# Performance work log

Measured on AMD Instinct MI355X. Metric: run time of the kernel, lower is better.

Reference implementation:

```python
import jax, jax.numpy as jnp
import numpy as np

DG = 4   # deformable groups
KK = 9   # 3x3 kernel
BN_EPS = 1e-5


def setup_inputs() -> dict:
    key = jax.random.key(0)
    ks = jax.random.split(key, 4)
    B, C, H, W = 4, 64, 160, 160
    fea = jax.random.normal(ks[0], (B, C, H, W), jnp.float32)
    # 1x1 offset conv (no bias) + BN (eval-mode running stats)
    w_off = jax.random.normal(ks[1], (C, C), jnp.float32) * 0.05
    bn_gamma = jnp.ones((C,), jnp.float32)
    bn_beta = jnp.zeros((C,), jnp.float32)
    bn_mean = jnp.zeros((C,), jnp.float32)
    bn_var = jnp.ones((C,), jnp.float32)
    # conv_offset_mask: 3x3 conv -> 3*DG*KK = 108 channels (o1, o2, mask)
    w_com = jax.random.normal(ks[2], (3 * DG * KK, C, 3, 3), jnp.float32) * 0.02
    b_com = jnp.zeros((3 * DG * KK,), jnp.float32)
    # modulated deformable conv main weight/bias
    w_dcn = jax.random.normal(ks[3], (C, C, 3, 3), jnp.float32) * 0.05
    b_dcn = jnp.zeros((C,), jnp.float32)
    return dict(fea=fea, w_off=w_off, bn_gamma=bn_gamma, bn_beta=bn_beta,
                bn_mean=bn_mean, bn_var=bn_var, w_com=w_com, b_com=b_com,
                w_dcn=w_dcn, b_dcn=b_dcn)


def _forward(fea, w_off, bn_gamma, bn_beta, bn_mean, bn_var, w_com, b_com, w_dcn, b_dcn):
    B, C, H, W = fea.shape
    Cg = C // DG
    # ---- offset branch: 1x1 conv + BN (eval) ----
    off_feat = jnp.einsum('bihw,oi->bohw', fea, w_off)
    inv = bn_gamma / jnp.sqrt(bn_var + BN_EPS)
    off_feat = off_feat * inv[None, :, None, None] + (bn_beta - bn_mean * inv)[None, :, None, None]
    # ---- conv_offset_mask 3x3, pad 1 ----
    com = jax.lax.conv_general_dilated(
        off_feat, w_com, (1, 1), ((1, 1), (1, 1)),
        dimension_numbers=('NCHW', 'OIHW', 'NCHW')) + b_com[None, :, None, None]
    o1, o2, m = jnp.split(com, 3, axis=1)                 # each [B, DG*KK, H, W]
    off = jnp.concatenate([o1, o2], axis=1).reshape(B, DG, KK, 2, H, W)
    dy = off[:, :, :, 0]                                  # [B, DG, KK, H, W]
    dx = off[:, :, :, 1]
    mask = jax.nn.sigmoid(m).reshape(B, DG, KK, H, W)
    # ---- sampling locations (stride=1, pad=1, dil=1) ----
    ky = (jnp.arange(KK) // 3 - 1).astype(fea.dtype)
    kx = (jnp.arange(KK) % 3 - 1).astype(fea.dtype)
    py = dy + ky[None, None, :, None, None] + jnp.arange(H, dtype=fea.dtype)[None, None, None, :, None]
    px = dx + kx[None, None, :, None, None] + jnp.arange(W, dtype=fea.dtype)[None, None, None, None, :]
    # ---- bilinear gather with zero padding outside ----
    fea_g = fea.reshape(B, DG, Cg, H * W)
    y0 = jnp.floor(py)
    x0 = jnp.floor(px)
    wy = py - y0
    wx = px - x0
    y0i = y0.astype(jnp.int32)
    x0i = x0.astype(jnp.int32)

    def corner(yi, xi, wgt):
        valid = ((yi >= 0) & (yi < H) & (xi >= 0) & (xi < W)).astype(fea.dtype)
        idx = jnp.clip(yi, 0, H - 1) * W + jnp.clip(xi, 0, W - 1)  # [B,DG,KK,H,W]
        v = jnp.take_along_axis(fea_g, idx.reshape(B, DG, 1, KK * H * W), axis=3)
        v = v.reshape(B, DG, Cg, KK, H, W)
        return v * (wgt * valid)[:, :, None]

    val = (corner(y0i,     x0i,     (1 - wy) * (1 - wx))
         + corner(y0i,     x0i + 1, (1 - wy) * wx)
         + corner(y0i + 1, x0i,     wy * (1 - wx))
         + corner(y0i + 1, x0i + 1, wy * wx))
    val = val * mask[:, :, None]                          # modulated im2col [B,DG,Cg,KK,H,W]
    # ---- deformable conv contraction + bias, relu, residual ----
    out = jnp.einsum('bgckhw,ogck->bohw', val, w_dcn.reshape(C, DG, Cg, KK)) + b_dcn[None, :, None, None]
    return fea + jax.nn.relu(out)


def reference(fea, w_off, bn_gamma, bn_beta, bn_mean, bn_var, w_com, b_com, w_dcn, b_dcn):
    return _forward(fea, w_off, bn_gamma, bn_beta, bn_mean, bn_var, w_com, b_com, w_dcn, b_dcn)
```

## Files before the change

kernel.cpp:

```cpp
#include <hip/hip_runtime.h>
#include <math.h>

#define Hc 160
#define Wc 160
#define HWc (Hc*Wc)
#define Cc 64
#define COMC 108

typedef __attribute__((ext_vector_type(8))) short short8;
typedef __attribute__((ext_vector_type(4))) float f32x4;
typedef __attribute__((ext_vector_type(2))) float f32x2;

__device__ inline short f2bf(float f) {
    union { float f; unsigned u; } v; v.f = f;
    unsigned r = (v.u + 0x7FFFu + ((v.u >> 16) & 1u)) >> 16;
    return (short)r;
}
__device__ inline float bf2f(short s) {
    union { unsigned u; float f; } v; v.u = ((unsigned)(unsigned short)s) << 16; return v.f;
}
__device__ inline float bflo(unsigned u) {
    union { unsigned u; float f; } v; v.u = u << 16; return v.f;
}
__device__ inline float bfhi(unsigned u) {
    union { unsigned u; float f; } v; v.u = u & 0xFFFF0000u; return v.f;
}
__device__ inline f32x2 bf2x2(unsigned u) {
    union { unsigned u; float f; } lo, hi;
    lo.u = u << 16; hi.u = u & 0xFFFF0000u;
    return (f32x2){lo.f, hi.f};
}
__device__ inline unsigned packbf_fast(float lo, float hi) {
    union { float f; unsigned u; } a, b; a.f = lo; b.f = hi;
    return ((a.u + 0x8000u) >> 16) | ((b.u + 0x8000u) & 0xFFFF0000u);
}

__global__ __launch_bounds__(256) void k_prep2(
    const float* __restrict__ w_off,
    const float* __restrict__ bn_g, const float* __restrict__ bn_b,
    const float* __restrict__ bn_m, const float* __restrict__ bn_v,
    const float* __restrict__ w_com, const float* __restrict__ w_dcn,
    short* __restrict__ wof_frag, float* __restrict__ shift,
    short* __restrict__ wfrag, short* __restrict__ wdT)
{
    const int t = blockIdx.x * 256 + threadIdx.x;
    if (t < 64) {
        const float scale = bn_g[t] * __frsqrt_rn(bn_v[t] + 1e-5f);
        shift[t] = bn_b[t] - bn_m[t] * scale;
    }
    if (t < 4096) {
        const int j = t & 7;
        const int lane = (t >> 3) & 63;
        const int v = t >> 9;
        const int s = v & 1, m = v >> 1;
        const int o = m*16 + (lane & 15);
        const int i = s*32 + (lane >> 4)*8 + j;
        const float scale = bn_g[o] * __frsqrt_rn(bn_v[o] + 1e-5f);
        wof_frag[t] = f2bf(w_off[o*64 + i] * scale);
    }
    if (t < 64512) {
        const int j = t & 7;
        const int lane = (t >> 3) & 63;
        const int v = t >> 9;
        const int s = v % 18, m = v / 18;
        const int kk = s >> 1, h = s & 1;
        const int o = m*16 + (lane & 15);
        const int i = h*32 + (lane >> 4)*8 + j;
        wfrag[t] = (o < COMC) ? f2bf(w_com[(o*64 + i)*9 + kk]) : (short)0;
    }
    if (t < 36864) {
        const int j = t & 7;
        const int lane = (t >> 3) & 63;
        const int v = t >> 9;
        const int s = v % 18, m = v / 18;
        const int o = m*16 + (lane & 15);
        const int q = s*32 + (lane >> 4)*8 + j;
        const int ch = q & 63, kk = q >> 6;
        wdT[t] = f2bf(w_dcn[o*576 + ch*9 + kk]);
    }
}

__global__ __launch_bounds__(256) void k_off3(
    const float* __restrict__ fea, const short* __restrict__ wof_frag,
    const float* __restrict__ shift,
    short* __restrict__ off_bf, short* __restrict__ fea_gp)
{
    __shared__ short sm[64][72];
    const int b = blockIdx.y;
    const int w = threadIdx.x >> 6, lane = threadIdx.x & 63;
    const int n = lane & 15, g = lane >> 4;
    const int p = blockIdx.x * 64 + w * 16 + n;
    const float* f = fea + (size_t)b * Cc * HWc + p;

    short8 bfrag[2];
    #pragma unroll
    for (int s = 0; s < 2; ++s) {
        #pragma unroll
        for (int j = 0; j < 8; ++j)
            bfrag[s][j] = f2bf(f[(size_t)(s*32 + g*8 + j) * HWc]);
        const int gg = s*2 + (g >> 1);
        *(short8*)&fea_gp[(((size_t)b*4 + gg)*HWc + p)*16 + (g & 1)*8] = bfrag[s];
    }

    f32x4 acc[4];
    #pragma unroll
    for (int m = 0; m < 4; ++m) acc[m] = (f32x4){0.f, 0.f, 0.f, 0.f};
    #pragma unroll
    for (int s = 0; s < 2; ++s) {
        #pragma unroll
        for (int m = 0; m < 4; ++m) {
            const short8 afrag = *(const short8*)&wof_frag[((m*2 + s)*64 + lane)*8];
            acc[m] = __builtin_amdgcn_mfma_f32_16x16x32_bf16(afrag, bfrag[s], acc[m], 0, 0, 0);
        }
    }
    #pragma unroll
    for (int m = 0; m < 4; ++m) {
        #pragma unroll
        for (int r = 0; r < 4; ++r) {
            const int o = m*16 + g*4 + r;
            sm[w*16 + n][o] = f2bf(acc[m][r] + shift[o]);
        }
    }
    __syncthreads();
    for (int q = threadIdx.x; q < 512; q += 256) {
        const int pl = q >> 3, sc = q & 7;
        *(uint4*)&off_bf[((size_t)(b * HWc) + blockIdx.x*64 + pl)*64 + sc*8] =
            *(const uint4*)&sm[pl][sc*8];
    }
}

#define SWZ(px, sc) ((sc) ^ ((px) & 7))

__global__ __launch_bounds__(256) void k_com6(
    const short* __restrict__ off_bf, const short* __restrict__ wfrag,
    const float* __restrict__ b_com, short* __restrict__ com_rec)
{
    __shared__ short smem[14336];
    const int seg = blockIdx.x;
    const int yb  = blockIdx.y * 4;
    const int b   = blockIdx.z;
    const int x0  = seg * 32;
    const int tid = threadIdx.x;

    for (int c = tid; c < 1632; c += 256) {
        const int r   = c / 272;
        const int rem = c - r * 272;
        const int px  = rem >> 3;
        const int sc  = rem & 7;
        const int gy  = yb + r - 1;
        const int gx  = x0 + px - 1;
        uint4 vv = make_uint4(0u, 0u, 0u, 0u);
        if ((unsigned)gy < (unsigned)Hc && (unsigned)gx < (unsigned)Wc)
            vv = *(const uint4*)&off_bf[(((size_t)b * HWc + gy * Wc + gx) << 6) + (sc << 3)];
        *(uint4*)&smem[((r*34 + px)*8 + SWZ(px, sc)) * 8] = vv;
    }
    __syncthreads();

    const int w    = tid >> 6;
    const int lane = tid & 63;
    const int n15  = lane & 15;
    const int g    = lane >> 4;
    const int m0   = w * 2;
    const int nm   = (w == 3) ? 1 : 2;

    f32x4 acc[2][8];
    #pragma unroll
    for (int mm = 0; mm < 2; ++mm)
        #pragma unroll
        for (int t = 0; t < 8; ++t) acc[mm][t] = (f32x4){0.f, 0.f, 0.f, 0.f};

    #pragma unroll
    for (int kk = 0; kk < 9; ++kk) {
        #pragma unroll
        for (int h = 0; h < 2; ++h) {
            const int s = kk*2 + h;
            const int slot = h*4 + g;
            short8 bf[8];
            #pragma unroll
            for (int t = 0; t < 8; ++t) {
                const int r  = t >> 1, xt = t & 1;
                const int ry = r + kk/3;
                const int rx = xt*16 + n15 + (kk % 3);
                bf[t] = *(const short8*)&smem[((ry*34 + rx)*8 + SWZ(rx, slot)) * 8];
            }
            #pragma unroll
            for (int mm = 0; mm < 2; ++mm) {
                if (mm < nm) {
                    const short8 afrag =
                        *(const short8*)&wfrag[(((m0+mm)*18 + s)*64 + lane)*8];
                    #pragma unroll
                    for (int t = 0; t < 8; ++t)
                        acc[mm][t] = __builtin_amdgcn_mfma_f32_16x16x32_bf16(
                            afrag, bf[t], acc[mm][t], 0, 0, 0);
                }
            }
        }
    }
    __syncthreads();

    #pragma unroll
    for (int mm = 0; mm < 2; ++mm) {
        if (mm < nm) {
            #pragma unroll
            for (int r4 = 0; r4 < 4; ++r4) {
                const int oc = (m0+mm)*16 + g*4 + r4;
                if (oc < COMC) {
                    int pos;
                    if (oc < 72) pos = oc;
                    else { const int q = oc - 72; pos = 72 + (q/9)*10 + (q - (q/9)*9); }
                    const float bo = b_com[oc];
                    #pragma unroll
                    for (int t = 0; t < 8; ++t) {
                        const int r = t >> 1, xt = t & 1;
                        smem[(r*32 + xt*16 + n15)*112 + pos] = f2bf(acc[mm][t][r4] + bo);
                    }
                }
            }
        }
    }
    __syncthreads();

    for (int c = tid; c < 1792; c += 256) {
        const int pr = c / 14, ch = c - pr * 14;
        const int r = pr >> 5, pxl = pr & 31;
        const int p = (yb + r) * Wc + x0 + pxl;
        *(uint4*)&com_rec[((size_t)b * HWc + p)*112 + ch*8] = *(const uint4*)&smem[pr*112 + ch*8];
    }
}

__global__ __launch_bounds__(256, 4) void k_dcn8(
    const float* __restrict__ fea, const short* __restrict__ com_rec,
    const short* __restrict__ fea_gp, const short* __restrict__ wdT,
    const float* __restrict__ b_dcn, float* __restrict__ out)
{
    __shared__ short stage_s[10752];
    __shared__ short val_s[9216];
    const int nx = gridDim.x;
    int bid = blockIdx.x;
    bid = (bid & 7) * (nx >> 3) + (bid >> 3);
    const int b = blockIdx.y;
    const int base = bid * 16;
    const int ty = base / Wc;
    const int tx = base - ty * Wc;
    const int tid = threadIdx.x;
    const int w = tid >> 6, lane = tid & 63;

    const int eo = tid >> 2, eq = tid & 3;
    const size_t egb = ((size_t)b * Cc + eo) * HWc + base + eq*4;
    const float4 fv = *(const float4*)&fea[egb];

    const int ns = (lane < 16) ? 3 : 2;
    int sk[3], sg[3], sl[3];
    unsigned sdydx[3]; float smk[3];
    #pragma unroll
    for (int i = 0; i < 3; ++i) {
        const int s = w*144 + i*64 + lane;
        sk[i] = s >> 6; sg[i] = (s >> 4) & 3; sl[i] = s & 15;
        if (i < ns) {
            const short* crp = &com_rec[((size_t)b * HWc + base + sl[i]) * 112];
            sdydx[i] = *(const unsigned*)&crp[sg[i]*18 + 2*sk[i]];
            smk[i]   = bf2f(crp[72 + sg[i]*10 + sk[i]]);
        }
    }

    for (int cq = tid; cq < 1344; cq += 256) {
        const int g = cq / 336, rem = cq - g*336;
        const int r = rem / 48, rem2 = rem - r*48;
        const int c = rem2 >> 1, h = rem2 & 1;
        const int gy = min(max(ty - 3 + r, 0), Hc-1);
        const int gx = min(max(tx - 3 + c, 0), Wc-1);
        *(uint4*)&stage_s[((g*7 + r)*24 + c)*16 + h*8] =
            *(const uint4*)&fea_gp[(((size_t)b*4 + g)*HWc + gy*Wc + gx)*16 + h*8];
    }
    __syncthreads();

    #pragma unroll
    for (int i = 0; i < 3; ++i) {
        if (i < ns) {
            const int k = sk[i], g = sg[i], lp = sl[i];
            const float dy = bflo(sdydx[i]), dx = bfhi(sdydx[i]);
            const float mk = 1.f / (1.f + __expf(-smk[i]));
            const float py  = dy + (float)(k/3 - 1 + ty);
            const float pxf = dx + (float)(k%3 - 1 + tx + lp);
            const float y0f = floorf(py), x0f = floorf(pxf);
            const float wy = py - y0f, wx = pxf - x0f;
            const int y0 = (int)y0f, x0i = (int)x0f;
            const int y1 = y0 + 1,  x1 = x0i + 1;
            const bool vy0 = (y0 >= 0) & (y0 < Hc);
            const bool vy1 = (y1 >= 0) & (y1 < Hc);
            const bool vx0 = (x0i >= 0) & (x0i < Wc);
            const bool vx1 = (x1 >= 0) & (x1 < Wc);
            const float c00 = (vy0 && vx0) ? (1.f-wy)*(1.f-wx)*mk : 0.f;
            const float c01 = (vy0 && vx1) ? (1.f-wy)*wx*mk       : 0.f;
            const float c10 = (vy1 && vx0) ? wy*(1.f-wx)*mk       : 0.f;
            const float c11 = (vy1 && vx1) ? wy*wx*mk             : 0.f;
            const int y0c = min(max(y0, 0), Hc-1), y1c = min(max(y1, 0), Hc-1);
            const int x0c = min(max(x0i, 0), Wc-1), x1c = min(max(x1, 0), Wc-1);
            const int wr0 = min(max(y0c - (ty-3), 0), 6);
            const int wr1 = min(max(y1c - (ty-3), 0), 6);
            const int wc0 = min(max(x0c - (tx-3), 0), 23);
            const int wc1 = min(max(x1c - (tx-3), 0), 23);
            const short* sgp = &stage_s[g*7*24*16];
            const short* r00 = sgp + ((wr0*24 + wc0) << 4);
            const short* r01 = sgp + ((wr0*24 + wc1) << 4);
            const short* r10 = sgp + ((wr1*24 + wc0) << 4);
            const short* r11 = sgp + ((wr1*24 + wc1) << 4);
            const uint4 a00 = *(const uint4*)r00, b00 = *(const uint4*)(r00 + 8);
            const uint4 a01 = *(const uint4*)r01, b01 = *(const uint4*)(r01 + 8);
            const uint4 a10 = *(const uint4*)r10, b10 = *(const uint4*)(r10 + 8);
            const uint4 a11 = *(const uint4*)r11, b11 = *(const uint4*)(r11 + 8);
            unsigned uo[8];
            {
                const unsigned* p00 = (const unsigned*)&a00;
                const unsigned* p01 = (const unsigned*)&a01;
                const unsigned* p10 = (const unsigned*)&a10;
                const unsigned* p11 = (const unsigned*)&a11;
                #pragma unroll
                for (int wi = 0; wi < 4; ++wi) {
                    const f32x2 v = bf2x2(p00[wi])*c00 + bf2x2(p01[wi])*c01
                                  + bf2x2(p10[wi])*c10 + bf2x2(p11[wi])*c11;
                    uo[wi] = packbf_fast(v.x, v.y);
                }
            }
            {
                const unsigned* p00 = (const unsigned*)&b00;
                const unsigned* p01 = (const unsigned*)&b01;
                const unsigned* p10 = (const unsigned*)&b10;
                const unsigned* p11 = (const unsigned*)&b11;
                #pragma unroll
                for (int wi = 0; wi < 4; ++wi) {
                    const f32x2 v = bf2x2(p00[wi])*c00 + bf2x2(p01[wi])*c01
                                  + bf2x2(p10[wi])*c10 + bf2x2(p11[wi])*c11;
                    uo[4 + wi] = packbf_fast(v.x, v.y);
                }
            }
            const int m7 = lp & 7;
            const int cc = k*8 + g*2;
            *(uint4*)&val_s[(lp*72 + ((cc    ) ^ m7)) * 8] = make_uint4(uo[0], uo[1], uo[2], uo[3]);
            *(uint4*)&val_s[(lp*72 + ((cc + 1) ^ m7)) * 8] = make_uint4(uo[4], uo[5], uo[6], uo[7]);
        }
    }
    __syncthreads();

    const int n  = lane & 15;
    const int g2 = lane >> 4;
    f32x4 acc = (f32x4){0.f, 0.f, 0.f, 0.f};
    const short* wp = wdT + ((w*18)*64 + lane)*8;
    #pragma unroll
    for (int s = 0; s < 18; ++s) {
        const int swz = (s*4 + g2) ^ (n & 7);
        const short8 bfrag = *(const short8*)&val_s[(n*72 + swz) * 8];
        const short8 afrag = *(const short8*)&wp[(s*64) * 8];
        acc = __builtin_amdgcn_mfma_f32_16x16x32_bf16(afrag, bfrag, acc, 0, 0, 0);
    }
    __syncthreads();
    float* ost = (float*)val_s;
    #pragma unroll
    for (int r = 0; r < 4; ++r) {
        const int o = w*16 + g2*4 + r;
        ost[o*17 + n] = acc[r] + b_dcn[o];
    }
    __syncthreads();

    float4 ov;
    ov.x = fv.x + fmaxf(ost[eo*17 + eq*4 + 0], 0.f);
    ov.y = fv.y + fmaxf(ost[eo*17 + eq*4 + 1], 0.f);
    ov.z = fv.z + fmaxf(ost[eo*17 + eq*4 + 2], 0.f);
    ov.w = fv.w + fmaxf(ost[eo*17 + eq*4 + 3], 0.f);
    *(float4*)&out[egb] = ov;
}

extern "C" void kernel_launch(void* const* d_in, const int* in_sizes, int n_in,
                              void* d_out, int out_size, void* d_ws, size_t ws_size,
                              hipStream_t stream) {
    const float* fea   = (const float*)d_in[0];
    const float* w_off = (const float*)d_in[1];
    const float* bn_g  = (const float*)d_in[2];
    const float* bn_b  = (const float*)d_in[3];
    const float* bn_m  = (const float*)d_in[4];
    const float* bn_v  = (const float*)d_in[5];
    const float* w_com = (const float*)d_in[6];
    const float* b_com = (const float*)d_in[7];
    const float* w_dcn = (const float*)d_in[8];
    const float* b_dcn = (const float*)d_in[9];
    float* out = (float*)d_out;

    char* ws = (char*)d_ws;
    short* com_rec  = (short*)ws;
    short* off_bf   = (short*)(ws + 22937600);
    short* fea_gp   = (short*)(ws + 36044800);
    short* wfrag    = (short*)(ws + 49152000);
    short* wdT      = (short*)(ws + 49281024);
    short* wof_frag = (short*)(ws + 49354752);
    float* shift    = (float*)(ws + 49362944);

    k_prep2<<<252, 256, 0, stream>>>(w_off, bn_g, bn_b, bn_m, bn_v,
                                     w_com, w_dcn, wof_frag, shift, wfrag, wdT);

    dim3 gA(HWc / 64, 4);
    k_off3<<<gA, 256, 0, stream>>>(fea, wof_frag, shift, off_bf, fea_gp);

    dim3 gB(5, Hc / 4, 4);
    k_com6<<<gB, 256, 0, stream>>>(off_bf, wfrag, b_com, com_rec);

    dim3 gC(HWc / 16, 4);
    k_dcn8<<<gC, 256, 0, stream>>>(fea, com_rec, fea_gp, wdT, b_dcn, out);
}
```

Measured before the change: 104.1 us.

## Restructure DCN kernel staging, val layout, and epilogue to drop LDS round-trip

```diff
diff --git a/kernel.cpp b/kernel.cpp
--- a/kernel.cpp
+++ b/kernel.cpp
@@ -30,9 +30,9 @@
     lo.u = u << 16; hi.u = u & 0xFFFF0000u;
     return (f32x2){lo.f, hi.f};
 }
-__device__ inline unsigned packbf_fast(float lo, float hi) {
-    union { float f; unsigned u; } a, b; a.f = lo; b.f = hi;
-    return ((a.u + 0x8000u) >> 16) | ((b.u + 0x8000u) & 0xFFFF0000u);
+__device__ inline unsigned packbf_perm(float lo, float hi) {
+    union { float f; unsigned u; } a, c; a.f = lo; c.f = hi;
+    return __builtin_amdgcn_perm(c.u + 0x8000u, a.u + 0x8000u, 0x07060302u);
 }
 
 __global__ __launch_bounds__(256) void k_prep2(
@@ -228,12 +228,15 @@
     }
 }
 
-__global__ __launch_bounds__(256, 4) void k_dcn8(
+#define SROW 360
+#define SG   (7*SROW)
+
+__global__ __launch_bounds__(256, 4) void k_dcn11(
     const float* __restrict__ fea, const short* __restrict__ com_rec,
     const short* __restrict__ fea_gp, const short* __restrict__ wdT,
     const float* __restrict__ b_dcn, float* __restrict__ out)
 {
-    __shared__ short stage_s[10752];
+    __shared__ short stage_s[4*SG];
     __shared__ short val_s[9216];
     const int nx = gridDim.x;
     int bid = blockIdx.x;
@@ -244,44 +247,53 @@
     const int tx = base - ty * Wc;
     const int tid = threadIdx.x;
     const int w = tid >> 6, lane = tid & 63;
-
-    const int eo = tid >> 2, eq = tid & 3;
-    const size_t egb = ((size_t)b * Cc + eo) * HWc + base + eq*4;
-    const float4 fv = *(const float4*)&fea[egb];
-
-    const int ns = (lane < 16) ? 3 : 2;
-    int sk[3], sg[3], sl[3];
+    const int n = lane & 15, g2 = lane >> 4;
+
+    const size_t outb = ((size_t)b * Cc + (w*16 + g2*4)) * HWc + base + n;
+    float resv[4], biasv[4];
+    #pragma unroll
+    for (int r = 0; r < 4; ++r) {
+        resv[r]  = fea[outb + (size_t)r * HWc];
+        biasv[r] = b_dcn[w*16 + g2*4 + r];
+    }
+
+    const int ns = (w < 2) ? 3 : (w == 2 ? 2 : 1);
+    const int sbase = (w <= 2) ? w * 192 : 512;
+    int sk[3];
+    const int sg = (lane >> 4) & 3;
+    const int sl = lane & 15;
     unsigned sdydx[3]; float smk[3];
     #pragma unroll
     for (int i = 0; i < 3; ++i) {
-        const int s = w*144 + i*64 + lane;
-        sk[i] = s >> 6; sg[i] = (s >> 4) & 3; sl[i] = s & 15;
+        sk[i] = (sbase + i*64 + lane) >> 6;
         if (i < ns) {
-            const short* crp = &com_rec[((size_t)b * HWc + base + sl[i]) * 112];
-            sdydx[i] = *(const unsigned*)&crp[sg[i]*18 + 2*sk[i]];
-            smk[i]   = bf2f(crp[72 + sg[i]*10 + sk[i]]);
-        }
-    }
-
-    for (int cq = tid; cq < 1344; cq += 256) {
-        const int g = cq / 336, rem = cq - g*336;
-        const int r = rem / 48, rem2 = rem - r*48;
-        const int c = rem2 >> 1, h = rem2 & 1;
-        const int gy = min(max(ty - 3 + r, 0), Hc-1);
+            const short* crp = &com_rec[((size_t)b * HWc + base + sl) * 112];
+            sdydx[i] = *(const unsigned*)&crp[sg*18 + 2*sk[i]];
+            smk[i]   = bf2f(crp[72 + sg*10 + sk[i]]);
+        }
+    }
+
+    if (lane < 44) {
+        const int c = lane >> 1, h = lane & 1;
         const int gx = min(max(tx - 3 + c, 0), Wc-1);
-        *(uint4*)&stage_s[((g*7 + r)*24 + c)*16 + h*8] =
-            *(const uint4*)&fea_gp[(((size_t)b*4 + g)*HWc + gy*Wc + gx)*16 + h*8];
+        const short* src = fea_gp + (((size_t)b*4 + w)*HWc)*16;
+        #pragma unroll
+        for (int r = 0; r < 7; ++r) {
+            const int gy = min(max(ty - 3 + r, 0), Hc-1);
+            *(uint4*)&stage_s[w*SG + r*SROW + c*16 + h*8] =
+                *(const uint4*)&src[(gy*Wc + gx)*16 + h*8];
+        }
     }
     __syncthreads();
 
     #pragma unroll
     for (int i = 0; i < 3; ++i) {
         if (i < ns) {
-            const int k = sk[i], g = sg[i], lp = sl[i];
+            const int k = sk[i];
             const float dy = bflo(sdydx[i]), dx = bfhi(sdydx[i]);
             const float mk = 1.f / (1.f + __expf(-smk[i]));
             const float py  = dy + (float)(k/3 - 1 + ty);
-            const float pxf = dx + (float)(k%3 - 1 + tx + lp);
+            const float pxf = dx + (float)(k%3 - 1 + tx + sl);
             const float y0f = floorf(py), x0f = floorf(pxf);
             const float wy = py - y0f, wx = pxf - x0f;
             const int y0 = (int)y0f, x0i = (int)x0f;
@@ -298,13 +310,13 @@
             const int x0c = min(max(x0i, 0), Wc-1), x1c = min(max(x1, 0), Wc-1);
             const int wr0 = min(max(y0c - (ty-3), 0), 6);
             const int wr1 = min(max(y1c - (ty-3), 0), 6);
-            const int wc0 = min(max(x0c - (tx-3), 0), 23);
-            const int wc1 = min(max(x1c - (tx-3), 0), 23);
-            const short* sgp = &stage_s[g*7*24*16];
-            const short* r00 = sgp + ((wr0*24 + wc0) << 4);
-            const short* r01 = sgp + ((wr0*24 + wc1) << 4);
-            const short* r10 = sgp + ((wr1*24 + wc0) << 4);
-            const short* r11 = sgp + ((wr1*24 + wc1) << 4);
+            const int wc0 = min(max(x0c - (tx-3), 0), 21);
+            const int wc1 = min(max(x1c - (tx-3), 0), 21);
+            const short* sgp = &stage_s[sg*SG];
+            const short* r00 = sgp + wr0*SROW + wc0*16;
+            const short* r01 = sgp + wr0*SROW + wc1*16;
+            const short* r10 = sgp + wr1*SROW + wc0*16;
+            const short* r11 = sgp + wr1*SROW + wc1*16;
             const uint4 a00 = *(const uint4*)r00, b00 = *(const uint4*)(r00 + 8);
             const uint4 a01 = *(const uint4*)r01, b01 = *(const uint4*)(r01 + 8);
             const uint4 a10 = *(const uint4*)r10, b10 = *(const uint4*)(r10 + 8);
@@ -319,7 +331,7 @@
                 for (int wi = 0; wi < 4; ++wi) {
                     const f32x2 v = bf2x2(p00[wi])*c00 + bf2x2(p01[wi])*c01
                                   + bf2x2(p10[wi])*c10 + bf2x2(p11[wi])*c11;
-                    uo[wi] = packbf_fast(v.x, v.y);
+                    uo[wi] = packbf_perm(v.x, v.y);
                 }
             }
             {
@@ -331,43 +343,29 @@
                 for (int wi = 0; wi < 4; ++wi) {
                     const f32x2 v = bf2x2(p00[wi])*c00 + bf2x2(p01[wi])*c01
                                   + bf2x2(p10[wi])*c10 + bf2x2(p11[wi])*c11;
-                    uo[4 + wi] = packbf_fast(v.x, v.y);
+                    uo[4 + wi] = packbf_perm(v.x, v.y);
                 }
             }
-            const int m7 = lp & 7;
-            const int cc = k*8 + g*2;
-            *(uint4*)&val_s[(lp*72 + ((cc    ) ^ m7)) * 8] = make_uint4(uo[0], uo[1], uo[2], uo[3]);
-            *(uint4*)&val_s[(lp*72 + ((cc + 1) ^ m7)) * 8] = make_uint4(uo[4], uo[5], uo[6], uo[7]);
-        }
-    }
-    __syncthreads();
-
-    const int n  = lane & 15;
-    const int g2 = lane >> 4;
+            const int cc = k*8 + sg*2;
+            *(uint4*)&val_s[((cc    )*16 + sl) * 8] = make_uint4(uo[0], uo[1], uo[2], uo[3]);
+            *(uint4*)&val_s[((cc + 1)*16 + sl) * 8] = make_uint4(uo[4], uo[5], uo[6], uo[7]);
+        }
+    }
+    __syncthreads();
+
     f32x4 acc = (f32x4){0.f, 0.f, 0.f, 0.f};
     const short* wp = wdT + ((w*18)*64 + lane)*8;
+    __builtin_amdgcn_s_setprio(1);
     #pragma unroll
     for (int s = 0; s < 18; ++s) {
-        const int swz = (s*4 + g2) ^ (n & 7);
-        const short8 bfrag = *(const short8*)&val_s[(n*72 + swz) * 8];
+        const short8 bfrag = *(const short8*)&val_s[((s*4 + g2)*16 + n) * 8];
         const short8 afrag = *(const short8*)&wp[(s*64) * 8];
         acc = __builtin_amdgcn_mfma_f32_16x16x32_bf16(afrag, bfrag, acc, 0, 0, 0);
     }
-    __syncthreads();
-    float* ost = (float*)val_s;
-    #pragma unroll
-    for (int r = 0; r < 4; ++r) {
-        const int o = w*16 + g2*4 + r;
-        ost[o*17 + n] = acc[r] + b_dcn[o];
-    }
-    __syncthreads();
-
-    float4 ov;
-    ov.x = fv.x + fmaxf(ost[eo*17 + eq*4 + 0], 0.f);
-    ov.y = fv.y + fmaxf(ost[eo*17 + eq*4 + 1], 0.f);
-    ov.z = fv.z + fmaxf(ost[eo*17 + eq*4 + 2], 0.f);
-    ov.w = fv.w + fmaxf(ost[eo*17 + eq*4 + 3], 0.f);
-    *(float4*)&out[egb] = ov;
+    __builtin_amdgcn_s_setprio(0);
+    #pragma unroll
+    for (int r = 0; r < 4; ++r)
+        out[outb + (size_t)r * HWc] = resv[r] + fmaxf(acc[r] + biasv[r], 0.f);
 }
 
 extern "C" void kernel_launch(void* const* d_in, const int* in_sizes, int n_in,
@@ -404,5 +402,5 @@
     k_com6<<<gB, 256, 0, stream>>>(off_bf, wfrag, b_com, com_rec);
 
     dim3 gC(HWc / 16, 4);
-    k_dcn8<<<gC, 256, 0, stream>>>(fea, com_rec, fea_gp, wdT, b_dcn, out);
-}
+    k_dcn11<<<gC, 256, 0, stream>>>(fea, com_rec, fea_gp, wdT, b_dcn, out);
+}
```

After: 97.77 us, median of 2. -6.1%, faster.
